# Performance work log

Measured on AMD Instinct MI355X. Metric: run time of the kernel, lower is better.

Reference implementation:

```python
import jax, jax.numpy as jnp
import numpy as np

B, T, E, V, L = 16, 500, 1024, 4000, 100
BLANK = 0
NEG = -1e30  # safe 'log zero' for float32


def setup_inputs() -> dict:
    key = jax.random.key(0)
    k1, k2, k3, k4, k5 = jax.random.split(key, 5)
    hs = jax.random.normal(k1, (B, T, E), dtype=jnp.float32)
    W = jax.random.normal(k2, (E, V), dtype=jnp.float32) * 0.02
    b = jnp.zeros((V,), dtype=jnp.float32)
    ys = jax.random.randint(k3, (B, L), 1, V, dtype=jnp.int32)  # labels exclude blank=0
    ilens = jax.random.randint(k4, (B,), T // 2, T + 1, dtype=jnp.int32)
    olens = jax.random.randint(k5, (B,), L // 2, L + 1, dtype=jnp.int32)
    # mark labels past olen as padding (-1), as F.pad_sequence(ys, padding=-1) would
    ys = jnp.where(jnp.arange(L)[None, :] < olens[:, None], ys, -1)
    return {"hs": hs, "W": W, "b": b, "ys": ys, "ilens": ilens, "olens": olens}


def _ctc_loss(lp, ys, ilens, olens):
    # lp: [B,T,V] log-probs; standard CTC forward DP in log space.
    Bn, Tn, Vn = lp.shape
    Ln = ys.shape[1]
    S = 2 * Ln + 1  # extended label length (blanks interleaved)
    ysc = jnp.where(ys < 0, BLANK, ys)
    ext = jnp.zeros((Bn, S), dtype=ys.dtype).at[:, 1::2].set(ysc)  # [B,S]
    prev2 = jnp.concatenate([jnp.full((Bn, 2), -1, ext.dtype), ext[:, :-2]], axis=1)
    allow_skip = (ext != BLANK) & (ext != prev2)  # s -> s-2 transition allowed
    # gather per-step emission log-probs for extended labels: [B,T,S]
    lp_ext = jnp.take_along_axis(lp, ext[:, None, :], axis=2)

    alpha0 = (jnp.full((Bn, S), NEG, lp.dtype)
              .at[:, 0].set(lp_ext[:, 0, 0])
              .at[:, 1].set(lp_ext[:, 0, 1]))

    def step(alpha, inp):
        lp_t, valid = inp  # lp_t: [B,S], valid: [B] (t < ilen)
        a1 = alpha
        a2 = jnp.concatenate([jnp.full((Bn, 1), NEG, alpha.dtype), alpha[:, :-1]], axis=1)
        a3 = jnp.concatenate([jnp.full((Bn, 2), NEG, alpha.dtype), alpha[:, :-2]], axis=1)
        a3 = jnp.where(allow_skip, a3, NEG)
        new = jnp.logaddexp(jnp.logaddexp(a1, a2), a3) + lp_t
        new = jnp.where(valid[:, None], new, alpha)  # freeze past ilen
        return new, None

    ts = jnp.arange(1, Tn)
    valid = ts[:, None] < ilens[None, :]            # [T-1, B]
    lp_seq = jnp.moveaxis(lp_ext[:, 1:, :], 1, 0)   # [T-1, B, S]
    alpha_T, _ = jax.lax.scan(step, alpha0, (lp_seq, valid))

    batch = jnp.arange(Bn)
    ll = jnp.logaddexp(alpha_T[batch, 2 * olens], alpha_T[batch, 2 * olens - 1])
    return -jnp.mean(ll)


def reference(hs, W, b, ys, ilens, olens):
    # dropout_rate = 0.0 -> identity; linear_tensor == dense over last dim
    logits = jnp.einsum('bte,ev->btv', hs, W) + b
    lp = jax.nn.log_softmax(logits, axis=-1)
    return _ctc_loss(lp, ys, ilens, olens)
```

## Files before the change

kernel.cpp:

```cpp
#include <hip/hip_runtime.h>

typedef unsigned short u16;
typedef unsigned int u32;
typedef unsigned char u8;
typedef __attribute__((ext_vector_type(4))) int int4v;
typedef __attribute__((ext_vector_type(8))) int int8v;
typedef __attribute__((ext_vector_type(4))) float f32x4;

#define NEG (-1e30f)
#define LN2 0.6931471805599453f
#define INV_LN2 1.4426950408889634f

#define B_N 16
#define T_N 500
#define E_N 1024
#define V_N 4000
#define L_N 100
#define M_P 8064
#define N_P 4096

#define PAIRS_B 128000UL
#define PB_OFF  128000UL
#define CT_OFF  130048UL
#define BSTRIDE 132096UL

#define OFF_A   0UL
#define OFF_B   8257536UL
#define OFF_C   12451840UL
#define OFF_LAB 78512128UL

__device__ __forceinline__ u16 f2bf(float f) {
  u32 u = __float_as_uint(f);
  u += 0x7fffu + ((u >> 16) & 1u);
  return (u16)(u >> 16);
}
__device__ __forceinline__ float bf2f(u16 h) {
  return __uint_as_float(((u32)h) << 16);
}
__device__ __forceinline__ void gl_lds16(const void* g, void* l) {
  __builtin_amdgcn_global_load_lds((const __attribute__((address_space(1))) void*)g,
                                   (__attribute__((address_space(3))) void*)l, 16, 0, 0);
}
template <int CTRL>
__device__ __forceinline__ float dpp_f(float x, float fill) {
  return __int_as_float(__builtin_amdgcn_update_dpp(
      __float_as_int(fill), __float_as_int(x), CTRL, 0xF, 0xF, false));
}
__device__ __forceinline__ float dpp_shr1(float x, float fill) {
  return dpp_f<0x138>(x, fill);
}
__device__ __forceinline__ float wave_max(float x, float fill) {
  x = fmaxf(x, dpp_f<0x111>(x, fill));
  x = fmaxf(x, dpp_f<0x112>(x, fill));
  x = fmaxf(x, dpp_f<0x114>(x, fill));
  x = fmaxf(x, dpp_f<0x118>(x, fill));
  x = fmaxf(x, dpp_f<0x142>(x, fill));
  x = fmaxf(x, dpp_f<0x143>(x, fill));
  return x;
}
__device__ __forceinline__ float wave_sum(float x) {
  x += dpp_f<0x111>(x, 0.f); x += dpp_f<0x112>(x, 0.f);
  x += dpp_f<0x114>(x, 0.f); x += dpp_f<0x118>(x, 0.f);
  x += dpp_f<0x142>(x, 0.f); x += dpp_f<0x143>(x, 0.f);
  return x;
}

__global__ __launch_bounds__(256) void castA(const float* __restrict__ hs,
                                             u32* __restrict__ Aq,
                                             float* __restrict__ out) {
  int idx = blockIdx.x * 256 + threadIdx.x;
  if (idx == 0) out[0] = 0.f;
  int row = idx >> 8;
  float4 x;
  if (row < B_N * T_N) x = ((const float4*)hs)[idx];
  else x = make_float4(0.f, 0.f, 0.f, 0.f);
  u32 p = __builtin_amdgcn_cvt_pk_fp8_f32(x.x, x.y, 0, false);
  p = __builtin_amdgcn_cvt_pk_fp8_f32(x.z, x.w, p, true);
  Aq[idx] = p;
}

__global__ __launch_bounds__(256) void castB(const float* __restrict__ W,
                                             u8* __restrict__ Bq) {
  __shared__ float tile[32][33];
  int v0 = blockIdx.x * 32;
  int e0 = blockIdx.y * 32;
  int tx = threadIdx.x & 31, ty = threadIdx.x >> 5;
#pragma unroll
  for (int i = 0; i < 4; ++i) {
    int e = e0 + ty * 4 + i;
    int v = v0 + tx;
    tile[ty * 4 + i][tx] = (v < V_N) ? W[e * V_N + v] : 0.f;
  }
  __syncthreads();
#pragma unroll
  for (int i = 0; i < 4; ++i) {
    int vloc = ty * 4 + i;
    float x = tile[tx][vloc] * 64.f;
    u32 p = __builtin_amdgcn_cvt_pk_fp8_f32(x, x, 0, false);
    Bq[(size_t)(v0 + vloc) * 1024 + (e0 + tx)] = (u8)(p & 0xff);
  }
}

__global__ __launch_bounds__(256, 2) void gemm_fp8(const u8* __restrict__ A,
                                                   const u8* __restrict__ Bq,
                                                   u16* __restrict__ C) {
  __shared__ __align__(16) u8 As[16 * 1056];
  __shared__ __align__(16) u8 Bs[16 * 1056];
  const int tid = threadIdx.x;
  const int lane = tid & 63;
  const int w = tid >> 6;
  const int wm = w >> 1, wn = w & 1;
  const size_t m0 = (size_t)blockIdx.y * 128;
  const size_t n0 = (size_t)blockIdx.x * 128;

  const int lr = lane >> 3;
  const int lc = lane & 7;
  const int gc = lc ^ lr;
  const u8* gA = A + (m0 + w * 32 + lr) * 1024 + gc * 16;
  const u8* gB = Bq + (n0 + w * 32 + lr) * 1024 + gc * 16;
  u8* sA = As + (w * 4) * 1056;
  u8* sB = Bs + (w * 4) * 1056;

  f32x4 acc[4][4];
#pragma unroll
  for (int i = 0; i < 4; ++i)
#pragma unroll
    for (int j = 0; j < 4; ++j) acc[i][j] = (f32x4){0.f, 0.f, 0.f, 0.f};

  const int fr = lane & 15, q = lane >> 4;
  const int c0 = ((2 * q) ^ (fr & 7)) * 16;
  const int c1 = ((2 * q + 1) ^ (fr & 7)) * 16;
  const int rA0 = wm * 64 + fr;
  const int rB0 = wn * 64 + fr;

  for (int kt = 0; kt < 1024; kt += 128) {
#pragma unroll
    for (int u = 0; u < 4; ++u) {
      gl_lds16(gA + (size_t)u * 8192 + kt, sA + u * 1056);
      gl_lds16(gB + (size_t)u * 8192 + kt, sB + u * 1056);
    }
    __syncthreads();
    int8v af[4], bf[4];
#pragma unroll
    for (int i = 0; i < 4; ++i) {
      int r = rA0 + i * 16;
      const u8* p = As + (r >> 3) * 1056 + (r & 7) * 128;
      int4v lo = *(const int4v*)(p + c0);
      int4v hi = *(const int4v*)(p + c1);
      af[i] = (int8v){lo[0], lo[1], lo[2], lo[3], hi[0], hi[1], hi[2], hi[3]};
    }
#pragma unroll
    for (int j = 0; j < 4; ++j) {
      int r = rB0 + j * 16;
      const u8* p = Bs + (r >> 3) * 1056 + (r & 7) * 128;
      int4v lo = *(const int4v*)(p + c0);
      int4v hi = *(const int4v*)(p + c1);
      bf[j] = (int8v){lo[0], lo[1], lo[2], lo[3], hi[0], hi[1], hi[2], hi[3]};
    }
#pragma unroll
    for (int i = 0; i < 4; ++i)
#pragma unroll
      for (int j = 0; j < 4; ++j)
        acc[i][j] = __builtin_amdgcn_mfma_scale_f32_16x16x128_f8f6f4(
            af[i], bf[j], acc[i][j], 0, 0,
            0, 0x7F7F7F7F, 0, 0x7F7F7F7F);
    __syncthreads();
  }

  const int cq = lane >> 4, cc = lane & 15;
#pragma unroll
  for (int i = 0; i < 4; ++i)
#pragma unroll
    for (int j = 0; j < 4; ++j) {
      size_t rr = m0 + wm * 64 + i * 16 + cq * 4;
      size_t nn = n0 + wn * 64 + j * 16 + cc;
      u16* o = C + rr * N_P + nn;
#pragma unroll
      for (int g = 0; g < 4; ++g) o[(size_t)g * N_P] = f2bf(acc[i][j][g] * 0.015625f);
    }
}

__global__ __launch_bounds__(256) void rowstat(const u16* __restrict__ C,
                                               const float* __restrict__ bias,
                                               const int* __restrict__ ys,
                                               u8* __restrict__ labbase) {
  int r = blockIdx.x;
  int tid = threadIdx.x;
  const u16* row = C + (size_t)r * N_P;
  int b = r / T_N;
  int t = r - b * T_N;
  float v[16];
  float mx = NEG;
#pragma unroll
  for (int u = 0; u < 16; ++u) {
    int c = tid + (u << 8);
    float x = (c < V_N) ? bf2f(row[c]) + bias[c] : NEG;
    v[u] = x;
    mx = fmaxf(mx, x);
  }
#pragma unroll
  for (int o = 32; o > 0; o >>= 1) mx = fmaxf(mx, __shfl_xor(mx, o));
  __shared__ float sm[4], ss[4];
  __shared__ float arr[104];
  __shared__ float cbr;
  int w = tid >> 6;
  if ((tid & 63) == 0) sm[w] = mx;
  __syncthreads();
  mx = fmaxf(fmaxf(sm[0], sm[1]), fmaxf(sm[2], sm[3]));
  float s = 0.f;
#pragma unroll
  for (int u = 0; u < 16; ++u) s += __expf(v[u] - mx);
#pragma unroll
  for (int o = 32; o > 0; o >>= 1) s += __shfl_xor(s, o);
  if ((tid & 63) == 0) ss[w] = s;
  __syncthreads();
  float lse = mx + __logf(ss[0] + ss[1] + ss[2] + ss[3]);

  if (tid <= 100) {
    int lab_id = (tid == 0) ? 0 : max(ys[b * L_N + tid - 1], 0);
    arr[tid] = (bf2f(row[lab_id]) + bias[lab_id] - lse) * INV_LN2;
  } else if (tid <= 103) {
    arr[tid] = NEG;
  }
  __syncthreads();
  if (tid < 64) {
    float vv = fmaxf(arr[tid], (tid < 40) ? arr[tid + 64] : NEG);
    vv = wave_max(vv, NEG);
    if (tid == 63) cbr = vv;
  }
  __syncthreads();
  float c = cbr;

  u8* base = labbase + (size_t)b * BSTRIDE;
  if (tid < 64) {
    float p0 = (tid < 50) ? exp2f(arr[1 + 2 * tid] - c) : 0.f;
    float p1 = (tid < 50) ? exp2f(arr[2 + 2 * tid] - c) : 0.f;
    u32 pk = ((u32)f2bf(p1) << 16) | (u32)f2bf(p0);
    ((u32*)base)[(size_t)t * 64 + tid] = pk;
  } else if (tid == 64) {
    ((float*)(base + PB_OFF))[t] = exp2f(arr[0] - c);
    ((float*)(base + CT_OFF))[t] = c;
  }
}

__global__ __launch_bounds__(64) void ctc_dp(const u8* __restrict__ labbase,
                                             const int* __restrict__ ys,
                                             const int* __restrict__ ilens,
                                             const int* __restrict__ olens,
                                             float* __restrict__ out) {
  __shared__ __align__(16) u8 sP[128000];
  __shared__ __align__(16) u8 sPBb[2048];
  __shared__ __align__(16) u8 sCTb[2048];
  int b = blockIdx.x;
  int L = threadIdx.x;
  const u8* gb = labbase + (size_t)b * BSTRIDE;

#pragma unroll 5
  for (int i = 0; i < 125; ++i)
    gl_lds16(gb + (size_t)i * 1024 + L * 16, sP + i * 1024);
  gl_lds16(gb + PB_OFF + L * 16, sPBb);
  gl_lds16(gb + PB_OFF + 1024 + L * 16, sPBb + 1024);
  gl_lds16(gb + CT_OFF + L * 16, sCTb);
  gl_lds16(gb + CT_OFF + 1024 + L * 16, sCTb + 1024);

  int k0 = 2 * L, k1 = 2 * L + 1;
  int k0c = min(k0, L_N - 1), k1c = min(k1, L_N - 1);
  int y0 = max(ys[b * L_N + k0c], 0);
  int y1 = max(ys[b * L_N + k1c], 0);
  int y0m = (k0 > 0) ? max(ys[b * L_N + min(k0 - 1, L_N - 1)], 0) : -1;
  bool allow1 = (y0 != 0) && (y0 != y0m);
  bool allow3 = (y1 != 0) && (y1 != y0);
  int il = ilens[b];

  asm volatile("s_waitcnt vmcnt(0)" ::: "memory");

  const u32* P = (const u32*)sP;
  const float* PB = (const float*)sPBb;
  const float* CT = (const float*)sCTb;

  float a0 = 0.f, a1 = 0.f, a2 = 0.f, a3 = 0.f;
  {
    float pb0 = PB[0];
    u32 pk00 = P[0];
    float a1v = __uint_as_float((pk00 & 0xffffu) << 16);
    if (L == 0) { a0 = pb0; a1 = a1v; }
  }
  int accE = 0;

  u32 curP[8]; float curB[8];
#pragma unroll
  for (int u = 0; u < 8; ++u) {
    curP[u] = P[(1 + u) * 64 + L];
    curB[u] = PB[1 + u];
  }
  for (int t0 = 1; t0 < il; t0 += 8) {
    u32 nP[8]; float nB[8];
#pragma unroll
    for (int u = 0; u < 8; ++u) {
      int tn = min(t0 + 8 + u, T_N - 1);
      nP[u] = P[tn * 64 + L];
      nB[u] = PB[tn];
    }
#pragma unroll
    for (int u = 0; u < 8; ++u) {
      int t = t0 + u;
      float pk0 = __uint_as_float((curP[u] & 0xffffu) << 16);
      float pk1 = __uint_as_float(curP[u] & 0xffff0000u);
      float p3 = dpp_shr1(a3, 0.f);
      float p3m = allow1 ? p3 : 0.f;
      float a1m = allow3 ? a1 : 0.f;
      float n0 = (a0 + p3) * curB[u];
      float n1 = (a1 + a0 + p3m) * pk0;
      float n2 = (a2 + a1) * curB[u];
      float n3 = (a3 + a2 + a1m) * pk1;
      bool live = t < il;
      a0 = live ? n0 : a0; a1 = live ? n1 : a1;
      a2 = live ? n2 : a2; a3 = live ? n3 : a3;
    }
    float m = fmaxf(fmaxf(a0, a1), fmaxf(a2, a3));
    m = wave_max(m, 0.f);
    u32 mb = (u32)__builtin_amdgcn_readlane(__float_as_int(m), 63);
    int ex = (int)((mb >> 23) & 0xffu);
    ex = (ex < 1) ? 1 : ex;
    float scale = __uint_as_float((u32)(254 - ex) << 23);
    a0 *= scale; a1 *= scale; a2 *= scale; a3 *= scale;
    accE += ex - 127;
#pragma unroll
    for (int u = 0; u < 8; ++u) { curP[u] = nP[u]; curB[u] = nB[u]; }
  }

  float cs = 0.f;
#pragma unroll
  for (int i = 0; i < 8; ++i) {
    int t = L + 64 * i;
    cs += (t < il) ? CT[t] : 0.f;
  }
  cs = wave_sum(cs);
  float csum = __int_as_float(__builtin_amdgcn_readlane(__float_as_int(cs), 63));

  int ol = olens[b];
  int s1 = 2 * ol, s2 = 2 * ol - 1;
  int j1 = s1 & 3, j2 = s2 & 3;
  float t1 = (j1 == 0) ? a0 : a2;
  float t2 = (j2 == 1) ? a1 : a3;
  float x1 = __shfl(t1, s1 >> 2);
  float x2 = __shfl(t2, s2 >> 2);
  float ll2 = __log2f(x1 + x2) + (float)accE + csum;
  if (L == 0) atomicAdd(out, -ll2 * LN2 * (1.0f / B_N));
}

extern "C" void kernel_launch(void* const* d_in, const int* in_sizes, int n_in,
                              void* d_out, int out_size, void* d_ws, size_t ws_size,
                              hipStream_t stream) {
  const float* hs    = (const float*)d_in[0];
  const float* W     = (const float*)d_in[1];
  const float* bias  = (const float*)d_in[2];
  const int*   ys    = (const int*)d_in[3];
  const int*   ilens = (const int*)d_in[4];
  const int*   olens = (const int*)d_in[5];
  char* ws = (char*)d_ws;
  u8*    Aq  = (u8*)(ws + OFF_A);
  u8*    Bq  = (u8*)(ws + OFF_B);
  u16*   C   = (u16*)(ws + OFF_C);
  u8*    lab = (u8*)(ws + OFF_LAB);
  float* out = (float*)d_out;

  castA<<<M_P * E_N / (256 * 4), 256, 0, stream>>>(hs, (u32*)Aq, out);
  castB<<<dim3(N_P / 32, E_N / 32), 256, 0, stream>>>(W, Bq);
  gemm_fp8<<<dim3(N_P / 128, M_P / 128), 256, 0, stream>>>(Aq, Bq, C);
  rowstat<<<B_N * T_N, 256, 0, stream>>>(C, bias, ys, lab);
  ctc_dp<<<B_N, 64, 0, stream>>>(lab, ys, ilens, olens, out);
}
```

Before: 192.6 us.

## Fuse softmax partial sums and label gather into GEMM epilogue, drop logits buffer

The GEMM epilogue now computes per-tile exp2 partial row sums and writes out the raw label-column logits, so the full bf16 logits matrix and the separate rowstat kernel are gone. The two cast kernels are merged into one launch. ctc_dp is widened to 512 threads and builds the normalized label probabilities in LDS from the partials before running the DP on a single wave. Exponentials are taken without max subtraction, which risks overflow for large logits. The label scatter loop in the epilogue adds per-block serial work.

```diff
diff --git a/kernel.cpp b/kernel.cpp
--- a/kernel.cpp
+++ b/kernel.cpp
@@ -19,15 +19,10 @@
 #define M_P 8064
 #define N_P 4096
 
-#define PAIRS_B 128000UL
-#define PB_OFF  128000UL
-#define CT_OFF  130048UL
-#define BSTRIDE 132096UL
-
 #define OFF_A   0UL
 #define OFF_B   8257536UL
-#define OFF_C   12451840UL
-#define OFF_LAB 78512128UL
+#define OFF_P   12451840UL
+#define OFF_LR  14516224UL
 
 __device__ __forceinline__ u16 f2bf(float f) {
   u32 u = __float_as_uint(f);
@@ -48,6 +43,11 @@
 }
 __device__ __forceinline__ float dpp_shr1(float x, float fill) {
   return dpp_f<0x138>(x, fill);
+}
+__device__ __forceinline__ float row16_sum(float x) {
+  x += dpp_f<0x111>(x, 0.f); x += dpp_f<0x112>(x, 0.f);
+  x += dpp_f<0x114>(x, 0.f); x += dpp_f<0x118>(x, 0.f);
+  return x;
 }
 __device__ __forceinline__ float wave_max(float x, float fill) {
   x = fmaxf(x, dpp_f<0x111>(x, fill));
@@ -65,53 +65,68 @@
   return x;
 }
 
-__global__ __launch_bounds__(256) void castA(const float* __restrict__ hs,
-                                             u32* __restrict__ Aq,
-                                             float* __restrict__ out) {
-  int idx = blockIdx.x * 256 + threadIdx.x;
-  if (idx == 0) out[0] = 0.f;
-  int row = idx >> 8;
-  float4 x;
-  if (row < B_N * T_N) x = ((const float4*)hs)[idx];
-  else x = make_float4(0.f, 0.f, 0.f, 0.f);
-  u32 p = __builtin_amdgcn_cvt_pk_fp8_f32(x.x, x.y, 0, false);
-  p = __builtin_amdgcn_cvt_pk_fp8_f32(x.z, x.w, p, true);
-  Aq[idx] = p;
-}
-
-__global__ __launch_bounds__(256) void castB(const float* __restrict__ W,
-                                             u8* __restrict__ Bq) {
+__global__ __launch_bounds__(256) void castAB(const float* __restrict__ hs,
+                                              const float* __restrict__ W,
+                                              u32* __restrict__ Aq,
+                                              u8* __restrict__ Bq,
+                                              float* __restrict__ out) {
   __shared__ float tile[32][33];
-  int v0 = blockIdx.x * 32;
-  int e0 = blockIdx.y * 32;
-  int tx = threadIdx.x & 31, ty = threadIdx.x >> 5;
-#pragma unroll
-  for (int i = 0; i < 4; ++i) {
-    int e = e0 + ty * 4 + i;
-    int v = v0 + tx;
-    tile[ty * 4 + i][tx] = (v < V_N) ? W[e * V_N + v] : 0.f;
-  }
-  __syncthreads();
-#pragma unroll
-  for (int i = 0; i < 4; ++i) {
-    int vloc = ty * 4 + i;
-    float x = tile[tx][vloc] * 64.f;
-    u32 p = __builtin_amdgcn_cvt_pk_fp8_f32(x, x, 0, false);
-    Bq[(size_t)(v0 + vloc) * 1024 + (e0 + tx)] = (u8)(p & 0xff);
+  if (blockIdx.x < 8064) {
+    int idx = blockIdx.x * 256 + threadIdx.x;
+    if (idx == 0) out[0] = 0.f;
+    int row = idx >> 8;
+    float4 x;
+    if (row < B_N * T_N) x = ((const float4*)hs)[idx];
+    else x = make_float4(0.f, 0.f, 0.f, 0.f);
+    u32 p = __builtin_amdgcn_cvt_pk_fp8_f32(x.x, x.y, 0, false);
+    p = __builtin_amdgcn_cvt_pk_fp8_f32(x.z, x.w, p, true);
+    Aq[idx] = p;
+  } else {
+    int bid = blockIdx.x - 8064;
+    int v0 = (bid & 127) * 32;
+    int e0 = (bid >> 7) * 32;
+    int tx = threadIdx.x & 31, ty = threadIdx.x >> 5;
+#pragma unroll
+    for (int i = 0; i < 4; ++i) {
+      int e = e0 + ty * 4 + i;
+      int v = v0 + tx;
+      tile[ty * 4 + i][tx] = (v < V_N) ? W[e * V_N + v] : 0.f;
+    }
+    __syncthreads();
+#pragma unroll
+    for (int i = 0; i < 4; ++i) {
+      int vloc = ty * 4 + i;
+      float x = tile[tx][vloc] * 64.f;
+      u32 p = __builtin_amdgcn_cvt_pk_fp8_f32(x, x, 0, false);
+      Bq[(size_t)(v0 + vloc) * 1024 + (e0 + tx)] = (u8)(p & 0xff);
+    }
   }
 }
 
 __global__ __launch_bounds__(256, 2) void gemm_fp8(const u8* __restrict__ A,
                                                    const u8* __restrict__ Bq,
-                                                   u16* __restrict__ C) {
+                                                   const float* __restrict__ bias,
+                                                   const int* __restrict__ ys,
+                                                   float* __restrict__ partial,
+                                                   float* __restrict__ labraw) {
   __shared__ __align__(16) u8 As[16 * 1056];
   __shared__ __align__(16) u8 Bs[16 * 1056];
+  __shared__ int extL2[2][104];
   const int tid = threadIdx.x;
   const int lane = tid & 63;
   const int w = tid >> 6;
   const int wm = w >> 1, wn = w & 1;
   const size_t m0 = (size_t)blockIdx.y * 128;
   const size_t n0 = (size_t)blockIdx.x * 128;
+
+  const int b0 = (int)m0 / 500;
+  const int b1 = min((int)m0 + 127, B_N * T_N - 1) / 500;
+  if (tid < 101)
+    extL2[0][tid] = (tid == 0) ? 0 : max(ys[b0 * L_N + tid - 1], 0);
+  else if (tid >= 128 && tid < 229) {
+    int t2 = tid - 128;
+    extL2[1][t2] = (t2 == 0) ? 0 : max(ys[b1 * L_N + t2 - 1], 0);
+  }
 
   const int lr = lane >> 3;
   const int lc = lane & 7;
@@ -168,121 +183,117 @@
   }
 
   const int cq = lane >> 4, cc = lane & 15;
-#pragma unroll
-  for (int i = 0; i < 4; ++i)
-#pragma unroll
-    for (int j = 0; j < 4; ++j) {
-      size_t rr = m0 + wm * 64 + i * 16 + cq * 4;
-      size_t nn = n0 + wn * 64 + j * 16 + cc;
-      u16* o = C + rr * N_P + nn;
-#pragma unroll
-      for (int g = 0; g < 4; ++g) o[(size_t)g * N_P] = f2bf(acc[i][j][g] * 0.015625f);
-    }
-}
-
-__global__ __launch_bounds__(256) void rowstat(const u16* __restrict__ C,
-                                               const float* __restrict__ bias,
-                                               const int* __restrict__ ys,
-                                               u8* __restrict__ labbase) {
-  int r = blockIdx.x;
+  const float K1C = 0.015625f * INV_LN2;
+  float k2j[4];
+#pragma unroll
+  for (int j = 0; j < 4; ++j) {
+    int col = (int)n0 + wn * 64 + j * 16 + cc;
+    k2j[j] = (col < V_N) ? bias[col] * INV_LN2 : -1e38f;
+  }
+#pragma unroll
+  for (int i = 0; i < 4; ++i) {
+    float sred[4];
+#pragma unroll
+    for (int g = 0; g < 4; ++g) {
+      float e0 = exp2f(acc[i][0][g] * K1C + k2j[0]);
+      float e1 = exp2f(acc[i][1][g] * K1C + k2j[1]);
+      float e2 = exp2f(acc[i][2][g] * K1C + k2j[2]);
+      float e3 = exp2f(acc[i][3][g] * K1C + k2j[3]);
+      sred[g] = row16_sum((e0 + e1) + (e2 + e3));
+    }
+    if (cc == 15) {
+#pragma unroll
+      for (int g = 0; g < 4; ++g) {
+        int row = (int)m0 + wm * 64 + i * 16 + cq * 4 + g;
+        partial[(size_t)row * 64 + blockIdx.x * 2 + wn] = sred[g];
+      }
+    }
+  }
+  int nbat = (b1 != b0) ? 2 : 1;
+  for (int bi = 0; bi < nbat; ++bi) {
+    int bb = bi ? b1 : b0;
+    int tlo = max(bb * 500, (int)m0);
+    int thi = min(bb * 500 + 500, min((int)m0 + 128, B_N * T_N));
+    float* lrb = labraw + (size_t)bb * 500 * 104;
+    for (int s = 0; s <= 100; ++s) {
+      int v = extL2[bi][s];
+      int lo = v - (int)n0 - wn * 64;
+      if (lo >= 0 && lo < 64) {
+        int jj = lo >> 4, ccv = lo & 15;
+        if (cc == ccv) {
+          float badd = bias[v] * INV_LN2;
+#pragma unroll
+          for (int j = 0; j < 4; ++j) {
+            if (j == jj) {
+#pragma unroll
+              for (int i = 0; i < 4; ++i)
+#pragma unroll
+                for (int g = 0; g < 4; ++g) {
+                  int row = (int)m0 + wm * 64 + i * 16 + cq * 4 + g;
+                  if (row >= tlo && row < thi)
+                    lrb[(size_t)(row - bb * 500) * 104 + s] =
+                        acc[i][j][g] * K1C + badd;
+                }
+            }
+          }
+        }
+      }
+    }
+  }
+}
+
+__global__ __launch_bounds__(512) void ctc_dp(const float* __restrict__ partial,
+                                              const float* __restrict__ labraw,
+                                              const int* __restrict__ ys,
+                                              const int* __restrict__ ilens,
+                                              const int* __restrict__ olens,
+                                              float* __restrict__ out) {
+  __shared__ __align__(16) u32 sP[500 * 64];
+  __shared__ float sPB[512];
+  __shared__ float sCT[512];
+  __shared__ int extL[104];
+  __shared__ float tmp[8][128];
+  int b = blockIdx.x;
   int tid = threadIdx.x;
-  const u16* row = C + (size_t)r * N_P;
-  int b = r / T_N;
-  int t = r - b * T_N;
-  float v[16];
-  float mx = NEG;
-#pragma unroll
-  for (int u = 0; u < 16; ++u) {
-    int c = tid + (u << 8);
-    float x = (c < V_N) ? bf2f(row[c]) + bias[c] : NEG;
-    v[u] = x;
-    mx = fmaxf(mx, x);
-  }
-#pragma unroll
-  for (int o = 32; o > 0; o >>= 1) mx = fmaxf(mx, __shfl_xor(mx, o));
-  __shared__ float sm[4], ss[4];
-  __shared__ float arr[104];
-  __shared__ float cbr;
-  int w = tid >> 6;
-  if ((tid & 63) == 0) sm[w] = mx;
+  int w = tid >> 6, L = tid & 63;
+
+  if (tid < 101) extL[tid] = (tid == 0) ? 0 : max(ys[b * L_N + tid - 1], 0);
+
+  const float* pbase = partial + (size_t)b * 500 * 64;
+  const float* lbase = labraw + (size_t)b * 500 * 104;
+  for (int t = w; t < T_N; t += 8) {
+    float S = wave_sum(pbase[t * 64 + L]);
+    float lse2 = __log2f(__int_as_float(
+        __builtin_amdgcn_readlane(__float_as_int(S), 63)));
+    float za = lbase[t * 104 + L] - lse2;
+    float zb = (L < 37) ? lbase[t * 104 + 64 + L] - lse2 : NEG;
+    float m = wave_max(fmaxf(za, zb), NEG);
+    float c = __int_as_float(__builtin_amdgcn_readlane(__float_as_int(m), 63));
+    float pa = exp2f(za - c);
+    float pb = (L < 37) ? exp2f(zb - c) : 0.f;
+    tmp[w][L] = pa;
+    if (L < 40) tmp[w][64 + L] = pb;
+    asm volatile("s_waitcnt lgkmcnt(0)" ::: "memory");
+    float p0 = (L < 50) ? tmp[w][1 + 2 * L] : 0.f;
+    float p1 = (L < 50) ? tmp[w][2 + 2 * L] : 0.f;
+    sP[t * 64 + L] = ((u32)f2bf(p1) << 16) | (u32)f2bf(p0);
+    if (L == 0) { sPB[t] = tmp[w][0]; sCT[t] = c; }
+  }
   __syncthreads();
-  mx = fmaxf(fmaxf(sm[0], sm[1]), fmaxf(sm[2], sm[3]));
-  float s = 0.f;
-#pragma unroll
-  for (int u = 0; u < 16; ++u) s += __expf(v[u] - mx);
-#pragma unroll
-  for (int o = 32; o > 0; o >>= 1) s += __shfl_xor(s, o);
-  if ((tid & 63) == 0) ss[w] = s;
-  __syncthreads();
-  float lse = mx + __logf(ss[0] + ss[1] + ss[2] + ss[3]);
-
-  if (tid <= 100) {
-    int lab_id = (tid == 0) ? 0 : max(ys[b * L_N + tid - 1], 0);
-    arr[tid] = (bf2f(row[lab_id]) + bias[lab_id] - lse) * INV_LN2;
-  } else if (tid <= 103) {
-    arr[tid] = NEG;
-  }
-  __syncthreads();
-  if (tid < 64) {
-    float vv = fmaxf(arr[tid], (tid < 40) ? arr[tid + 64] : NEG);
-    vv = wave_max(vv, NEG);
-    if (tid == 63) cbr = vv;
-  }
-  __syncthreads();
-  float c = cbr;
-
-  u8* base = labbase + (size_t)b * BSTRIDE;
-  if (tid < 64) {
-    float p0 = (tid < 50) ? exp2f(arr[1 + 2 * tid] - c) : 0.f;
-    float p1 = (tid < 50) ? exp2f(arr[2 + 2 * tid] - c) : 0.f;
-    u32 pk = ((u32)f2bf(p1) << 16) | (u32)f2bf(p0);
-    ((u32*)base)[(size_t)t * 64 + tid] = pk;
-  } else if (tid == 64) {
-    ((float*)(base + PB_OFF))[t] = exp2f(arr[0] - c);
-    ((float*)(base + CT_OFF))[t] = c;
-  }
-}
-
-__global__ __launch_bounds__(64) void ctc_dp(const u8* __restrict__ labbase,
-                                             const int* __restrict__ ys,
-                                             const int* __restrict__ ilens,
-                                             const int* __restrict__ olens,
-                                             float* __restrict__ out) {
-  __shared__ __align__(16) u8 sP[128000];
-  __shared__ __align__(16) u8 sPBb[2048];
-  __shared__ __align__(16) u8 sCTb[2048];
-  int b = blockIdx.x;
-  int L = threadIdx.x;
-  const u8* gb = labbase + (size_t)b * BSTRIDE;
-
-#pragma unroll 5
-  for (int i = 0; i < 125; ++i)
-    gl_lds16(gb + (size_t)i * 1024 + L * 16, sP + i * 1024);
-  gl_lds16(gb + PB_OFF + L * 16, sPBb);
-  gl_lds16(gb + PB_OFF + 1024 + L * 16, sPBb + 1024);
-  gl_lds16(gb + CT_OFF + L * 16, sCTb);
-  gl_lds16(gb + CT_OFF + 1024 + L * 16, sCTb + 1024);
+  if (w != 0) return;
 
   int k0 = 2 * L, k1 = 2 * L + 1;
-  int k0c = min(k0, L_N - 1), k1c = min(k1, L_N - 1);
-  int y0 = max(ys[b * L_N + k0c], 0);
-  int y1 = max(ys[b * L_N + k1c], 0);
-  int y0m = (k0 > 0) ? max(ys[b * L_N + min(k0 - 1, L_N - 1)], 0) : -1;
+  int y0 = extL[1 + min(k0, L_N - 1)];
+  int y1 = extL[1 + min(k1, L_N - 1)];
+  int y0m = (k0 > 0) ? extL[1 + min(k0 - 1, L_N - 1)] : -1;
   bool allow1 = (y0 != 0) && (y0 != y0m);
   bool allow3 = (y1 != 0) && (y1 != y0);
   int il = ilens[b];
 
-  asm volatile("s_waitcnt vmcnt(0)" ::: "memory");
-
-  const u32* P = (const u32*)sP;
-  const float* PB = (const float*)sPBb;
-  const float* CT = (const float*)sCTb;
-
   float a0 = 0.f, a1 = 0.f, a2 = 0.f, a3 = 0.f;
   {
-    float pb0 = PB[0];
-    u32 pk00 = P[0];
-    float a1v = __uint_as_float((pk00 & 0xffffu) << 16);
+    float pb0 = sPB[0];
+    float a1v = bf2f((u16)(sP[0] & 0xffffu));
     if (L == 0) { a0 = pb0; a1 = a1v; }
   }
   int accE = 0;
@@ -290,16 +301,16 @@
   u32 curP[8]; float curB[8];
 #pragma unroll
   for (int u = 0; u < 8; ++u) {
-    curP[u] = P[(1 + u) * 64 + L];
-    curB[u] = PB[1 + u];
+    curP[u] = sP[(1 + u) * 64 + L];
+    curB[u] = sPB[1 + u];
   }
   for (int t0 = 1; t0 < il; t0 += 8) {
     u32 nP[8]; float nB[8];
 #pragma unroll
     for (int u = 0; u < 8; ++u) {
       int tn = min(t0 + 8 + u, T_N - 1);
-      nP[u] = P[tn * 64 + L];
-      nB[u] = PB[tn];
+      nP[u] = sP[tn * 64 + L];
+      nB[u] = sPB[tn];
     }
 #pragma unroll
     for (int u = 0; u < 8; ++u) {
@@ -333,7 +344,7 @@
 #pragma unroll
   for (int i = 0; i < 8; ++i) {
     int t = L + 64 * i;
-    cs += (t < il) ? CT[t] : 0.f;
+    cs += (t < il) ? sCT[t] : 0.f;
   }
   cs = wave_sum(cs);
   float csum = __int_as_float(__builtin_amdgcn_readlane(__float_as_int(cs), 63));
@@ -359,15 +370,14 @@
   const int*   ilens = (const int*)d_in[4];
   const int*   olens = (const int*)d_in[5];
   char* ws = (char*)d_ws;
-  u8*    Aq  = (u8*)(ws + OFF_A);
-  u8*    Bq  = (u8*)(ws + OFF_B);
-  u16*   C   = (u16*)(ws + OFF_C);
-  u8*    lab = (u8*)(ws + OFF_LAB);
-  float* out = (float*)d_out;
-
-  castA<<<M_P * E_N / (256 * 4), 256, 0, stream>>>(hs, (u32*)Aq, out);
-  castB<<<dim3(N_P / 32, E_N / 32), 256, 0, stream>>>(W, Bq);
-  gemm_fp8<<<dim3(N_P / 128, M_P / 128), 256, 0, stream>>>(Aq, Bq, C);
-  rowstat<<<B_N * T_N, 256, 0, stream>>>(C, bias, ys, lab);
-  ctc_dp<<<B_N, 64, 0, stream>>>(lab, ys, ilens, olens, out);
-}
+  u8*    Aq   = (u8*)(ws + OFF_A);
+  u8*    Bq   = (u8*)(ws + OFF_B);
+  float* part = (float*)(ws + OFF_P);
+  float* lraw = (float*)(ws + OFF_LR);
+  float* out  = (float*)d_out;
+
+  castAB<<<12160, 256, 0, stream>>>(hs, W, (u32*)Aq, Bq, out);
+  gemm_fp8<<<dim3(N_P / 128, M_P / 128), 256, 0, stream>>>(Aq, Bq, bias, ys,
+                                                           part, lraw);
+  ctc_dp<<<B_N, 512, 0, stream>>>(part, lraw, ys, ilens, olens, out);
+}
```

Result: slower. 399.4 us (+107.4%).
